# Optimization experiments

Measured on AMD Instinct MI355X. Metric: run time of the kernel, lower is better.

Reference implementation:

```python
import jax, jax.numpy as jnp
import numpy as np

KH, KW = 3, 3
C_OUT = 32


def setup_inputs() -> dict:
    key = jax.random.key(0)
    k1, k2, k3 = jax.random.split(key, 3)
    B, H, W, C_IN = 32, 128, 128, 32
    P_DIM = 128
    X = jax.random.normal(k1, (B, H, W, C_IN), dtype=jnp.float32)
    P = jax.random.normal(k2, (B, P_DIM), dtype=jnp.float32)
    # hypernetwork Dense weight: p_dim -> kh*kw*c_in*c_out (no bias, no activation)
    dense_w = jax.random.normal(k3, (P_DIM, KH * KW * C_IN * C_OUT), dtype=jnp.float32) * 0.05
    return {"X": X, "P": P, "dense_w": dense_w}


def _conv_one(x, w):
    # x: [H, W, c_in], w: [kh, kw, c_in, c_out] -> [H, W, c_out], SAME padding, stride 1
    y = jax.lax.conv_general_dilated(
        x[None], w, window_strides=(1, 1), padding="SAME",
        dimension_numbers=("NHWC", "HWIO", "NHWC"))
    return y[0]


def reference(X, P, dense_w):
    B = X.shape[0]
    c_in = X.shape[-1]
    # hypernetwork: per-sample conv kernels
    A = P @ dense_w                              # [B, kh*kw*c_in*c_out]
    Wk = A.reshape(B, KH, KW, c_in, C_OUT)       # [B, kh, kw, c_in, c_out]
    # batched per-sample conv (equivalent to tf.map_fn over conv2d)
    return jax.vmap(_conv_one)(X, Wk)            # [B, H, W, c_out]
```

## Files before the change

### kernel.cpp

```cpp
#include <hip/hip_runtime.h>


#define BATCH 32
#define HDIM 128
#define WDIM 128
#define CIN 32
#define COUT 32
#define PDIM 128
#define KCOLS 9216

typedef _Float16 f16x8 __attribute__((ext_vector_type(8)));
typedef float f32x4 __attribute__((ext_vector_type(4)));

__device__ __forceinline__ f16x8 zero8() {
    f16x8 z;
#pragma unroll
    for (int j = 0; j < 8; ++j) z[j] = (_Float16)0.f;
    return z;
}

__global__ __launch_bounds__(256) void hyper_gemm(const float* __restrict__ P,
                                                  const float* __restrict__ Dw,
                                                  unsigned short* __restrict__ WB) {
    const int tid = threadIdx.x;
    const int lane = tid & 63;
    const int cg = blockIdx.x % 144;
    const int bq = blockIdx.x / 144;
    const int col = cg * 64 + lane;
    const int b0 = __builtin_amdgcn_readfirstlane(bq * 16 + (tid >> 6) * 4);
    const float* pb = P + (size_t)b0 * PDIM;

    float acc[4];
#pragma unroll
    for (int j = 0; j < 4; ++j) acc[j] = 0.f;

#pragma unroll 2
    for (int mm = 0; mm < PDIM; mm += 16) {
        float d[16];
#pragma unroll
        for (int u = 0; u < 16; ++u) d[u] = Dw[(size_t)(mm + u) * KCOLS + col];
#pragma unroll
        for (int u = 0; u < 16; ++u) {
#pragma unroll
            for (int j = 0; j < 4; ++j) acc[j] += d[u] * pb[j * PDIM + mm + u];
        }
    }

    const int co = col & 31;
    const int k = col >> 5;
    const int kc = k >> 5;
    const int ci = k & 31;
    const int base =
        ((kc * 2 + (co >> 4)) * 64 + (ci >> 3) * 16 + (co & 15)) * 8 + (ci & 7);
#pragma unroll
    for (int j = 0; j < 4; ++j) {
        _Float16 v = (_Float16)acc[j];
        WB[(size_t)(b0 + j) * KCOLS + base] = __builtin_bit_cast(unsigned short, v);
    }
}

__device__ __forceinline__ f16x8 halo_ld(const f32x4* __restrict__ gp, int px) {
    const bool ok = (unsigned)px < 128u;
    const int p = ok ? px : 0;
    f32x4 lo = gp[p * 8];
    f32x4 hi = gp[p * 8 + 1];
    f16x8 o;
#pragma unroll
    for (int j = 0; j < 4; ++j) {
        o[j] = (_Float16)lo[j];
        o[4 + j] = (_Float16)hi[j];
    }
    if (!ok) o = zero8();
    return o;
}

template <bool TOPG>
__device__ __forceinline__ void compute_group(const char* xsb, int ldsbase,
                                              const f16x8* bf, float* ybase,
                                              const f32x4* gp, bool gvalid,
                                              int wave, int q, int m16) {
    f16x8 hal[3];
    if (gvalid) {
#pragma unroll
        for (int kw = 0; kw < 3; ++kw) hal[kw] = halo_ld(gp, m16 + kw - 1);
    } else {
#pragma unroll
        for (int kw = 0; kw < 3; ++kw) hal[kw] = zero8();
    }

    int va[3];
#pragma unroll
    for (int kw = 0; kw < 3; ++kw) {
        const int px = m16 + kw - 1;
        const int sl = (q ^ (px >> 1)) & 3;
        va[kw] = ldsbase + (wave - 1) * 8192 + px * 64 + sl * 16;
    }

#pragma unroll
    for (int t = 0; t < 8; ++t) {
        f32x4 acc0 = {0.f, 0.f, 0.f, 0.f};
        f32x4 acc1 = {0.f, 0.f, 0.f, 0.f};

#pragma unroll
        for (int kh = 0; kh < 3; ++kh) {
            f16x8 a0, a1, a2;
            const bool use_lds = (kh == 1) || (kh == 0 && (!TOPG || wave != 0)) ||
                                 (kh == 2 && wave != 7);
            if (use_lds) {
                int v0 = va[0] + kh * 8192;
                int v1 = va[1] + kh * 8192;
                int v2 = va[2] + kh * 8192;
                if (t == 0) v0 += (m16 == 0) ? 64 : 0;
                if (t == 7) v2 -= (m16 == 15) ? 64 : 0;
                a0 = *(const f16x8*)(xsb + v0);
                a1 = *(const f16x8*)(xsb + v1);
                a2 = *(const f16x8*)(xsb + v2);
                if (t == 0 && m16 == 0) a0 = zero8();
                if (t == 7 && m16 == 15) a2 = zero8();
            } else {
                a0 = hal[0];
                a1 = hal[1];
                a2 = hal[2];
                if (gvalid && t < 7) {
#pragma unroll
                    for (int kw = 0; kw < 3; ++kw)
                        hal[kw] = halo_ld(gp, (t + 1) * 16 + m16 + kw - 1);
                }
            }
            acc0 = __builtin_amdgcn_mfma_f32_16x16x32_f16(a0, bf[(kh * 3 + 0) * 2], acc0, 0, 0, 0);
            acc1 = __builtin_amdgcn_mfma_f32_16x16x32_f16(a0, bf[(kh * 3 + 0) * 2 + 1], acc1, 0, 0, 0);
            acc0 = __builtin_amdgcn_mfma_f32_16x16x32_f16(a1, bf[(kh * 3 + 1) * 2], acc0, 0, 0, 0);
            acc1 = __builtin_amdgcn_mfma_f32_16x16x32_f16(a1, bf[(kh * 3 + 1) * 2 + 1], acc1, 0, 0, 0);
            acc0 = __builtin_amdgcn_mfma_f32_16x16x32_f16(a2, bf[(kh * 3 + 2) * 2], acc0, 0, 0, 0);
            acc1 = __builtin_amdgcn_mfma_f32_16x16x32_f16(a2, bf[(kh * 3 + 2) * 2 + 1], acc1, 0, 0, 0);
        }

        float* yp = ybase + t * 16 * COUT;
#pragma unroll
        for (int r = 0; r < 4; ++r) {
            yp[r * COUT] = acc0[r];
            yp[r * COUT + 16] = acc1[r];
        }

#pragma unroll
        for (int kw = 0; kw < 3; ++kw) va[kw] += 1024;
    }
}

__global__ __launch_bounds__(512, 2) void conv_fused(const float* __restrict__ X,
                                                     const unsigned short* __restrict__ WB,
                                                     float* __restrict__ Y) {
    __shared__ f16x8 Xs[16 * 512];
    const int tid = threadIdx.x;

    const int wg = blockIdx.x;
    const int id = (wg & 7) * 32 + (wg >> 3);
    const int b = id >> 3;
    const int hg = id & 7;
    const int r0 = hg * 16;

    const int wave = tid >> 6;
    const int lane = tid & 63;
    const int q = lane >> 4;
    const int m16 = lane & 15;

    f16x8 bf[18];
    {
        const f16x8* wbp = (const f16x8*)(WB + (size_t)b * KCOLS);
#pragma unroll
        for (int i = 0; i < 18; ++i) bf[i] = wbp[i * 64 + lane];
    }

    const int px_s = tid >> 2;
    const int q_s = tid & 3;
    const int g_s = px_s * 4 + ((q_s ^ (px_s >> 1)) & 3);
    const float* xsrc = X + (((size_t)b * HDIM + r0) * WDIM + px_s) * CIN + q_s * 8;

#pragma unroll
    for (int r = 0; r < 8; ++r) {
        f32x4 lo = *(const f32x4*)(xsrc + (size_t)r * WDIM * CIN);
        f32x4 hi = *(const f32x4*)(xsrc + (size_t)r * WDIM * CIN + 4);
        f16x8 o;
#pragma unroll
        for (int j = 0; j < 4; ++j) {
            o[j] = (_Float16)lo[j];
            o[4 + j] = (_Float16)hi[j];
        }
        Xs[r * 512 + g_s] = o;
    }

    f32x4 R[16];
    const float* xsrc1 = xsrc + (size_t)8 * WDIM * CIN;
#pragma unroll
    for (int r = 0; r < 8; ++r) {
        R[2 * r] = *(const f32x4*)(xsrc1 + (size_t)r * WDIM * CIN);
        R[2 * r + 1] = *(const f32x4*)(xsrc1 + (size_t)r * WDIM * CIN + 4);
    }

    __syncthreads();

    const char* xsb = (const char*)Xs;
    const f32x4* Xb = (const f32x4*)X + (size_t)b * HDIM * (WDIM * CIN / 4);

    {
        const bool gvalid = (wave == 0) ? (hg != 0) : (wave == 7);
        const int grow = (wave == 0) ? (hg ? r0 - 1 : 0) : (r0 + 8);
        const f32x4* gp = Xb + (size_t)grow * (WDIM * CIN / 4) + q * 2;
        float* yb = Y + (((size_t)b * HDIM + r0 + wave) * WDIM + q * 4) * COUT + m16;
        compute_group<true>(xsb, 0, bf, yb, gp, gvalid, wave, q, m16);
    }

#pragma unroll
    for (int r = 0; r < 8; ++r) {
        f16x8 o;
#pragma unroll
        for (int j = 0; j < 4; ++j) {
            o[j] = (_Float16)R[2 * r][j];
            o[4 + j] = (_Float16)R[2 * r + 1][j];
        }
        Xs[(8 + r) * 512 + g_s] = o;
    }
    __syncthreads();

    {
        const bool gvalid = (wave == 7) && (hg != 7);
        const int grow = gvalid ? (r0 + 16) : 0;
        const f32x4* gp = Xb + (size_t)grow * (WDIM * CIN / 4) + q * 2;
        float* yb = Y + (((size_t)b * HDIM + r0 + 8 + wave) * WDIM + q * 4) * COUT + m16;
        compute_group<false>(xsb, 8 * 8192, bf, yb, gp, gvalid, wave, q, m16);
    }
}

extern "C" void kernel_launch(void* const* d_in, const int* in_sizes, int n_in,
                              void* d_out, int out_size, void* d_ws, size_t ws_size,
                              hipStream_t stream) {
    const float* X = (const float*)d_in[0];
    const float* P = (const float*)d_in[1];
    const float* Dw = (const float*)d_in[2];
    float* Y = (float*)d_out;
    (void)ws_size;

    unsigned short* WB = (unsigned short*)d_ws;

    hipLaunchKernelGGL(hyper_gemm, dim3(288), dim3(256), 0, stream, P, Dw, WB);
    hipLaunchKernelGGL(conv_fused, dim3(256), dim3(512), 0, stream, X, WB, Y);
}
```

Measured before the change: 132.8 us.

## Stage conv weights in LDS and interleave second-half X prefetch with compute

Moves the per-sample conv weight fragments from 18 registers per lane into an LDS buffer shared by the workgroup, read per MFMA. The prefetch of the second eight input rows is also spread across the first compute loop's iterations instead of being issued up front. Together these cut vector register pressure and let the global loads overlap with MFMA work. The cost is extra LDS traffic and 18KB more shared memory per block, which may limit the two-blocks-per-CU target.

```diff
diff --git a/kernel.cpp b/kernel.cpp
--- a/kernel.cpp
+++ b/kernel.cpp
@@ -17,6 +17,16 @@
 #pragma unroll
     for (int j = 0; j < 8; ++j) z[j] = (_Float16)0.f;
     return z;
+}
+
+__device__ __forceinline__ f16x8 cvt8(f32x4 lo, f32x4 hi) {
+    f16x8 o;
+#pragma unroll
+    for (int j = 0; j < 4; ++j) {
+        o[j] = (_Float16)lo[j];
+        o[4 + j] = (_Float16)hi[j];
+    }
+    return o;
 }
 
 __global__ __launch_bounds__(256) void hyper_gemm(const float* __restrict__ P,
@@ -74,11 +84,12 @@
     return o;
 }
 
-template <bool TOPG>
+template <bool TOPG, bool PRE>
 __device__ __forceinline__ void compute_group(const char* xsb, int ldsbase,
-                                              const f16x8* bf, float* ybase,
+                                              const f16x8* bfl, float* ybase,
                                               const f32x4* gp, bool gvalid,
-                                              int wave, int q, int m16) {
+                                              int wave, int q, int m16,
+                                              f32x4* R, const float* xsrc1) {
     f16x8 hal[3];
     if (gvalid) {
 #pragma unroll
@@ -98,6 +109,11 @@
 
 #pragma unroll
     for (int t = 0; t < 8; ++t) {
+        if constexpr (PRE) {
+            R[2 * t] = *(const f32x4*)(xsrc1 + (size_t)t * WDIM * CIN);
+            R[2 * t + 1] = *(const f32x4*)(xsrc1 + (size_t)t * WDIM * CIN + 4);
+        }
+
         f32x4 acc0 = {0.f, 0.f, 0.f, 0.f};
         f32x4 acc1 = {0.f, 0.f, 0.f, 0.f};
 
@@ -127,12 +143,12 @@
                         hal[kw] = halo_ld(gp, (t + 1) * 16 + m16 + kw - 1);
                 }
             }
-            acc0 = __builtin_amdgcn_mfma_f32_16x16x32_f16(a0, bf[(kh * 3 + 0) * 2], acc0, 0, 0, 0);
-            acc1 = __builtin_amdgcn_mfma_f32_16x16x32_f16(a0, bf[(kh * 3 + 0) * 2 + 1], acc1, 0, 0, 0);
-            acc0 = __builtin_amdgcn_mfma_f32_16x16x32_f16(a1, bf[(kh * 3 + 1) * 2], acc0, 0, 0, 0);
-            acc1 = __builtin_amdgcn_mfma_f32_16x16x32_f16(a1, bf[(kh * 3 + 1) * 2 + 1], acc1, 0, 0, 0);
-            acc0 = __builtin_amdgcn_mfma_f32_16x16x32_f16(a2, bf[(kh * 3 + 2) * 2], acc0, 0, 0, 0);
-            acc1 = __builtin_amdgcn_mfma_f32_16x16x32_f16(a2, bf[(kh * 3 + 2) * 2 + 1], acc1, 0, 0, 0);
+            acc0 = __builtin_amdgcn_mfma_f32_16x16x32_f16(a0, bfl[((kh * 3 + 0) * 2 + 0) * 64], acc0, 0, 0, 0);
+            acc1 = __builtin_amdgcn_mfma_f32_16x16x32_f16(a0, bfl[((kh * 3 + 0) * 2 + 1) * 64], acc1, 0, 0, 0);
+            acc0 = __builtin_amdgcn_mfma_f32_16x16x32_f16(a1, bfl[((kh * 3 + 1) * 2 + 0) * 64], acc0, 0, 0, 0);
+            acc1 = __builtin_amdgcn_mfma_f32_16x16x32_f16(a1, bfl[((kh * 3 + 1) * 2 + 1) * 64], acc1, 0, 0, 0);
+            acc0 = __builtin_amdgcn_mfma_f32_16x16x32_f16(a2, bfl[((kh * 3 + 2) * 2 + 0) * 64], acc0, 0, 0, 0);
+            acc1 = __builtin_amdgcn_mfma_f32_16x16x32_f16(a2, bfl[((kh * 3 + 2) * 2 + 1) * 64], acc1, 0, 0, 0);
         }
 
         float* yp = ybase + t * 16 * COUT;
@@ -151,6 +167,7 @@
                                                      const unsigned short* __restrict__ WB,
                                                      float* __restrict__ Y) {
     __shared__ f16x8 Xs[16 * 512];
+    __shared__ f16x8 BFs[KCOLS / 8];
     const int tid = threadIdx.x;
 
     const int wg = blockIdx.x;
@@ -164,11 +181,9 @@
     const int q = lane >> 4;
     const int m16 = lane & 15;
 
-    f16x8 bf[18];
     {
         const f16x8* wbp = (const f16x8*)(WB + (size_t)b * KCOLS);
-#pragma unroll
-        for (int i = 0; i < 18; ++i) bf[i] = wbp[i * 64 + lane];
+        for (int i = tid; i < KCOLS / 8; i += 512) BFs[i] = wbp[i];
     }
 
     const int px_s = tid >> 2;
@@ -180,45 +195,28 @@
     for (int r = 0; r < 8; ++r) {
         f32x4 lo = *(const f32x4*)(xsrc + (size_t)r * WDIM * CIN);
         f32x4 hi = *(const f32x4*)(xsrc + (size_t)r * WDIM * CIN + 4);
-        f16x8 o;
-#pragma unroll
-        for (int j = 0; j < 4; ++j) {
-            o[j] = (_Float16)lo[j];
-            o[4 + j] = (_Float16)hi[j];
-        }
-        Xs[r * 512 + g_s] = o;
-    }
-
+        Xs[r * 512 + g_s] = cvt8(lo, hi);
+    }
+
+    __syncthreads();
+
+    const char* xsb = (const char*)Xs;
+    const f16x8* bfl = BFs + lane;
+    const f32x4* Xb = (const f32x4*)X + (size_t)b * HDIM * (WDIM * CIN / 4);
+    const float* xsrc1 = xsrc + (size_t)8 * WDIM * CIN;
     f32x4 R[16];
-    const float* xsrc1 = xsrc + (size_t)8 * WDIM * CIN;
-#pragma unroll
-    for (int r = 0; r < 8; ++r) {
-        R[2 * r] = *(const f32x4*)(xsrc1 + (size_t)r * WDIM * CIN);
-        R[2 * r + 1] = *(const f32x4*)(xsrc1 + (size_t)r * WDIM * CIN + 4);
-    }
-
-    __syncthreads();
-
-    const char* xsb = (const char*)Xs;
-    const f32x4* Xb = (const f32x4*)X + (size_t)b * HDIM * (WDIM * CIN / 4);
 
     {
         const bool gvalid = (wave == 0) ? (hg != 0) : (wave == 7);
         const int grow = (wave == 0) ? (hg ? r0 - 1 : 0) : (r0 + 8);
         const f32x4* gp = Xb + (size_t)grow * (WDIM * CIN / 4) + q * 2;
         float* yb = Y + (((size_t)b * HDIM + r0 + wave) * WDIM + q * 4) * COUT + m16;
-        compute_group<true>(xsb, 0, bf, yb, gp, gvalid, wave, q, m16);
+        compute_group<true, true>(xsb, 0, bfl, yb, gp, gvalid, wave, q, m16, R, xsrc1);
     }
 
 #pragma unroll
     for (int r = 0; r < 8; ++r) {
-        f16x8 o;
-#pragma unroll
-        for (int j = 0; j < 4; ++j) {
-            o[j] = (_Float16)R[2 * r][j];
-            o[4 + j] = (_Float16)R[2 * r + 1][j];
-        }
-        Xs[(8 + r) * 512 + g_s] = o;
+        Xs[(8 + r) * 512 + g_s] = cvt8(R[2 * r], R[2 * r + 1]);
     }
     __syncthreads();
 
@@ -227,7 +225,8 @@
         const int grow = gvalid ? (r0 + 16) : 0;
         const f32x4* gp = Xb + (size_t)grow * (WDIM * CIN / 4) + q * 2;
         float* yb = Y + (((size_t)b * HDIM + r0 + 8 + wave) * WDIM + q * 4) * COUT + m16;
-        compute_group<false>(xsb, 8 * 8192, bf, yb, gp, gvalid, wave, q, m16);
+        compute_group<false, false>(xsb, 8 * 8192, bfl, yb, gp, gvalid, wave, q, m16,
+                                    R, xsrc1);
     }
 }
 
```

After: 138.8 us. 1.05x slower.
